# Kernel tuning notes

Hardware: AMD Instinct MI355X
Metric: run time of the kernel (lower is better)

## Reference

```python
import jax, jax.numpy as jnp
import numpy as np

VOCAB = 50257
D = 256
BATCH = 8


def setup_inputs() -> dict:
    key = jax.random.key(0)
    k1, k2, k3, k4, k5 = jax.random.split(key, 5)
    initial_ids = jax.random.randint(k1, (BATCH, 1), 0, VOCAB, dtype=jnp.int32)
    state = jax.random.normal(k2, (BATCH, D), dtype=jnp.float32)
    emb = jax.random.normal(k3, (VOCAB, D), dtype=jnp.float32) * 0.02
    W = jax.random.normal(k4, (D, VOCAB), dtype=jnp.float32) * 0.02
    U = jax.random.normal(k5, (D, D), dtype=jnp.float32) * 0.02
    return {"initial_ids": initial_ids, "state": state, "emb": emb,
            "W": W, "U": U, "beam_size": 32, "max_decode_length": 16}


def _logits_fn(ids, state, emb, W, U):
    # Stand-in for the external logits_fn: simple tanh-RNN cell + vocab projection.
    # ids: [b, beam, L], state: [b, beam, d]
    last = ids[:, :, -1]                                       # [b, beam]
    x = jnp.tanh(jnp.einsum('bkd,de->bke', state, U) + emb[last])  # [b, beam, d]
    token_scores = jax.nn.log_softmax(jnp.einsum('bkd,dv->bkv', x, W), axis=-1)
    return token_scores, x


def reference(initial_ids, state, emb, W, U, beam_size, max_decode_length):
    b = initial_ids.shape[0]
    vocab = W.shape[1]
    ids = initial_ids[:, None, :]                # [b, 1, L0]  (beam0 = 1)
    cache = state[:, None, :]                    # [b, 1, d]
    scores = jnp.zeros((b, 1), dtype=jnp.float32)
    for i in range(max_decode_length):           # unrolled, as in the TF original
        beam0 = ids.shape[1]
        token_scores, cache = _logits_fn(ids, cache, emb, W, U)   # [b,beam0,V]
        k = min(beam_size, beam0 * vocab)
        all_scores = (scores[:, :, None] + token_scores).reshape(b, beam0 * vocab)
        top_scores, top_ixs = jax.lax.top_k(all_scores, k)        # sorted, [b,k]
        top_beams = top_ixs // vocab                              # [b,k]
        top_tokens = top_ixs % vocab                              # [b,k]
        ids = jnp.take_along_axis(ids, top_beams[:, :, None], axis=1)
        ids = jnp.concatenate([ids, top_tokens[:, :, None].astype(ids.dtype)], axis=-1)
        cache = jnp.take_along_axis(cache, top_beams[:, :, None], axis=1)
        scores = top_scores
    return ids, scores
```

## Files before the change

### kernel.cpp

```cpp
#include <hip/hip_runtime.h>
#include <math.h>

#define B 8
#define D 256
#define V 50257
#define VP 50304
#define BEAM 32
#define STEPS 16
#define MAXLEN 17
#define FNEG_INF (-3.4e38f)
#define NG 1571
#define NLCAP 800
#define SLOTCAP 1600

struct SchedT {
    int nl, nops, nlev, root;
    int lvlStart[36];
    int leafOff[NLCAP];
    int leafN[NLCAP];
    int sA[NLCAP];
    int sB[NLCAP];
    int sD[NLCAP];
};

constexpr SchedT build_sched() {
    SchedT s{};
    int sOff[64] = {}, sN[64] = {}, sPh[64] = {};
    int vSlot[64] = {}, vLev[64] = {};
    int oA[NLCAP] = {}, oB[NLCAP] = {}, oD[NLCAP] = {}, oL[NLCAP] = {};
    int sp = 0, vp = 0, nl = 0, nops = 0;
    sOff[0] = 0; sN[0] = V; sPh[0] = 0; sp = 1;
    while (sp) {
        int i = sp - 1;
        int n = sN[i];
        if (n <= 128) {
            s.leafOff[nl] = sOff[i]; s.leafN[nl] = n;
            vSlot[vp] = nl; vLev[vp] = 0; ++vp; ++nl; --sp; continue;
        }
        int n2 = (n / 2) - ((n / 2) % 8);
        int ph = sPh[i];
        if (ph == 0)      { sPh[i] = 1; sOff[sp] = sOff[i];      sN[sp] = n2;     sPh[sp] = 0; ++sp; }
        else if (ph == 1) { sPh[i] = 2; sOff[sp] = sOff[i] + n2; sN[sp] = n - n2; sPh[sp] = 0; ++sp; }
        else {
            int bI = --vp; int aI = --vp;
            int lev = (vLev[aI] > vLev[bI] ? vLev[aI] : vLev[bI]) + 1;
            oA[nops] = vSlot[aI]; oB[nops] = vSlot[bI]; oD[nops] = NLCAP + nops; oL[nops] = lev;
            vSlot[vp] = NLCAP + nops; vLev[vp] = lev; ++vp; ++nops; --sp;
        }
    }
    s.nl = nl; s.nops = nops; s.root = vSlot[0];
    int maxl = 0;
    for (int k = 0; k < nops; ++k) if (oL[k] > maxl) maxl = oL[k];
    s.nlev = maxl;
    int cnt[36] = {};
    for (int k = 0; k < nops; ++k) cnt[oL[k]]++;
    int run = 0;
    s.lvlStart[0] = 0;
    for (int k = 1; k <= maxl; ++k) { s.lvlStart[k] = run; run += cnt[k]; cnt[k] = s.lvlStart[k]; }
    s.lvlStart[maxl + 1] = run;
    for (int k = 0; k < nops; ++k) { int p = cnt[oL[k]]++; s.sA[p] = oA[k]; s.sB[p] = oB[k]; s.sD[p] = oD[k]; }
    return s;
}

constexpr SchedT SCH = build_sched();
static_assert(SCH.nl <= NLCAP, "leaf overflow");
static_assert(SCH.nops <= NLCAP, "op overflow");
static_assert(SCH.nlev <= 34, "level overflow");
static_assert(SCH.root < SLOTCAP, "slot overflow");

__global__ void k_init(const int* __restrict__ initial_ids, const float* __restrict__ state,
                       float* __restrict__ cache, int* __restrict__ ids, float* __restrict__ scores) {
    int b = blockIdx.x, t = threadIdx.x;
    cache[b * D + t] = state[b * D + t];
    if (t == 0) { ids[b * MAXLEN] = initial_ids[b]; scores[b] = 0.f; }
}

__global__ __launch_bounds__(256) void k_embed(const float* __restrict__ cache, const int* __restrict__ ids,
                                               const float* __restrict__ emb, const float* __restrict__ U,
                                               float* __restrict__ x, int step) {
    int rr = blockIdx.x, j = threadIdx.x;
    __shared__ float sc[D];
    sc[j] = cache[rr * D + j];
    __syncthreads();
    int last = ids[rr * MAXLEN + step];
    float acc = 0.f;
    for (int d = 0; d < D; ++d)
        acc = __fadd_rn(acc, __fmul_rn(sc[d], U[d * D + j]));
    float pre = __fadd_rn(acc, emb[(size_t)last * D + j]);
    x[rr * D + j] = (float)tanh((double)pre);
}

__global__ __launch_bounds__(256) void k_trans(const float* __restrict__ x, float* __restrict__ xT) {
    __shared__ float tile[32][33];
    int t = threadIdx.x;
    int tx = t & 31, ty = t >> 5;
    int bx = blockIdx.x * 32, by = blockIdx.y * 32;
#pragma unroll
    for (int i = 0; i < 4; ++i)
        tile[ty + i * 8][tx] = x[(size_t)(by + ty + i * 8) * D + bx + tx];
    __syncthreads();
#pragma unroll
    for (int i = 0; i < 4; ++i)
        xT[(size_t)(bx + ty + i * 8) * 256 + by + tx] = tile[tx][ty + i * 8];
}

__global__ __launch_bounds__(256) void k_gemm(const float* __restrict__ xT, const float* __restrict__ W,
                                              float* __restrict__ L, int rows) {
    int t = threadIdx.x;
    int v = blockIdx.x * 256 + t;
    int r0 = blockIdx.y * 32;
    if (v >= V) return;
    float acc[32];
#pragma unroll
    for (int r = 0; r < 32; ++r) acc[r] = 0.f;
    for (int d = 0; d < D; ++d) {
        float w = W[(size_t)d * V + v];
        const float* xp = xT + d * 256 + r0;
#pragma unroll
        for (int r = 0; r < 32; ++r)
            acc[r] = __fadd_rn(acc[r], __fmul_rn(xp[r], w));
    }
#pragma unroll
    for (int r = 0; r < 32; ++r)
        if (r0 + r < rows) L[(size_t)(r0 + r) * VP + v] = acc[r];
}

__device__ __forceinline__ float Ev(const float* __restrict__ a, float m, int i) {
    return (float)exp((double)__fsub_rn(a[i], m));
}
__device__ float leaf_sum(const float* __restrict__ a, int n, float m) {
    if (n < 8) {
        if (n <= 0) return 0.f;
        float r = Ev(a, m, 0);
        for (int i = 1; i < n; ++i) r = __fadd_rn(r, Ev(a, m, i));
        return r;
    }
    float r0 = Ev(a,m,0), r1 = Ev(a,m,1), r2 = Ev(a,m,2), r3 = Ev(a,m,3);
    float r4 = Ev(a,m,4), r5 = Ev(a,m,5), r6 = Ev(a,m,6), r7 = Ev(a,m,7);
    int i;
    for (i = 8; i < n - (n % 8); i += 8) {
        r0 = __fadd_rn(r0, Ev(a,m,i+0)); r1 = __fadd_rn(r1, Ev(a,m,i+1));
        r2 = __fadd_rn(r2, Ev(a,m,i+2)); r3 = __fadd_rn(r3, Ev(a,m,i+3));
        r4 = __fadd_rn(r4, Ev(a,m,i+4)); r5 = __fadd_rn(r5, Ev(a,m,i+5));
        r6 = __fadd_rn(r6, Ev(a,m,i+6)); r7 = __fadd_rn(r7, Ev(a,m,i+7));
    }
    float res = __fadd_rn(__fadd_rn(__fadd_rn(r0, r1), __fadd_rn(r2, r3)),
                          __fadd_rn(__fadd_rn(r4, r5), __fadd_rn(r6, r7)));
    for (; i < n; ++i) res = __fadd_rn(res, Ev(a,m,i));
    return res;
}

__global__ __launch_bounds__(512) void k_post(const float* __restrict__ L, const float* __restrict__ scores,
                                              float* __restrict__ candV, int* __restrict__ candI) {
    int rr = blockIdx.x, t = threadIdx.x;
    const float* Lr = L + (size_t)rr * VP;
    __shared__ float red[512];
    __shared__ int ri[512];
    __shared__ float vals[SLOTCAP];
    __shared__ float gval[NG]; __shared__ int gidx[NG]; __shared__ unsigned gmask[NG];

    float mx = FNEG_INF;
    const float4* L4 = (const float4*)Lr;
    for (int i = t; i < V / 4; i += 512) {
        float4 p = L4[i];
        mx = fmaxf(mx, fmaxf(fmaxf(p.x, p.y), fmaxf(p.z, p.w)));
    }
    if (t == 0) mx = fmaxf(mx, Lr[V - 1]);
    red[t] = mx; __syncthreads();
    for (int o = 256; o > 0; o >>= 1) { if (t < o) red[t] = fmaxf(red[t], red[t + o]); __syncthreads(); }
    float m = red[0];

    for (int l = t; l < SCH.nl; l += 512)
        vals[l] = leaf_sum(Lr + SCH.leafOff[l], SCH.leafN[l], m);
    __syncthreads();
    for (int lev = 1; lev <= SCH.nlev; ++lev) {
        for (int i = SCH.lvlStart[lev] + t; i < SCH.lvlStart[lev + 1]; i += 512)
            vals[SCH.sD[i]] = __fadd_rn(vals[SCH.sA[i]], vals[SCH.sB[i]]);
        __syncthreads();
    }
    float lsf = (float)log((double)vals[SCH.root]);
    float sc = scores[rr];

    for (int g = t; g < NG; g += 512) {
        int c0 = g * 32;
        int lim = (V - c0) < 32 ? (V - c0) : 32;
        float bv = FNEG_INF; int bi = 0x7fffffff;
        for (int c = 0; c < lim; ++c) {
            int vtok = c0 + c;
            float val = __fadd_rn(sc, __fsub_rn(__fsub_rn(Lr[vtok], m), lsf));
            if (val > bv) { bv = val; bi = vtok; }
        }
        gval[g] = bv; gidx[g] = bi; gmask[g] = 0u;
    }
    __syncthreads();

    for (int it = 0; it < 32; ++it) {
        float bv = FNEG_INF; int bi = 0x7fffffff;
        for (int g = t; g < NG; g += 512) {
            float gv = gval[g]; int gi = gidx[g];
            if (gv > bv || (gv == bv && gi < bi)) { bv = gv; bi = gi; }
        }
        red[t] = bv; ri[t] = bi; __syncthreads();
        for (int o = 256; o > 0; o >>= 1) {
            if (t < o) {
                if (red[t + o] > red[t] || (red[t + o] == red[t] && ri[t + o] < ri[t])) { red[t] = red[t + o]; ri[t] = ri[t + o]; }
            }
            __syncthreads();
        }
        int wcol = ri[0]; int wg = wcol >> 5;
        if (t == 0) {
            candV[rr * 32 + it] = red[0];
            candI[rr * 32 + it] = wcol;
            gmask[wg] |= (1u << (wcol & 31));
        }
        __syncthreads();
        if (t < 32) {
            int col = wg * 32 + t;
            unsigned msk = gmask[wg];
            bool live = (col < V) && !((msk >> t) & 1u);
            float val = live ? __fadd_rn(sc, __fsub_rn(__fsub_rn(Lr[col], m), lsf)) : FNEG_INF;
            int ix = live ? col : 0x7fffffff;
            for (int o = 16; o > 0; o >>= 1) {
                float v2 = __shfl_down(val, o, 32);
                int i2 = __shfl_down(ix, o, 32);
                if (v2 > val || (v2 == val && i2 < ix)) { val = v2; ix = i2; }
            }
            if (t == 0) { gval[wg] = val; gidx[wg] = ix; }
        }
        __syncthreads();
    }
}

__global__ __launch_bounds__(256) void k_merge(const float* __restrict__ candV, const int* __restrict__ candI,
                                               float* __restrict__ scoresNxt,
                                               const int* __restrict__ idsCur, int* __restrict__ idsNxt,
                                               const float* __restrict__ x, float* __restrict__ cacheNxt,
                                               int beam0, int step) {
    int b = blockIdx.x, t = threadIdx.x;
    int n = beam0 * BEAM;
    __shared__ float mval[BEAM * BEAM]; __shared__ int mbeam[BEAM * BEAM]; __shared__ int mtok[BEAM * BEAM];
    __shared__ float rv[256]; __shared__ int rk[256]; __shared__ int rs[256];
    __shared__ float wval[BEAM]; __shared__ int wbeam[BEAM]; __shared__ int wtok[BEAM];

    for (int i = t; i < n; i += 256) {
        int beam = i >> 5;
        int rr = b * beam0 + beam;
        mval[i] = candV[rr * BEAM + (i & 31)];
        mbeam[i] = beam;
        mtok[i] = candI[rr * BEAM + (i & 31)];
    }
    __syncthreads();

    for (int it = 0; it < BEAM; ++it) {
        float bv = FNEG_INF; int bk = 0x7fffffff; int bs = -1;
        for (int i = t; i < n; i += 256) {
            float v = mval[i];
            int gi = mbeam[i] * V + mtok[i];
            if (v > bv || (v == bv && gi < bk)) { bv = v; bk = gi; bs = i; }
        }
        rv[t] = bv; rk[t] = bk; rs[t] = bs; __syncthreads();
        for (int o = 128; o > 0; o >>= 1) {
            if (t < o) {
                if (rv[t + o] > rv[t] || (rv[t + o] == rv[t] && rk[t + o] < rk[t])) {
                    rv[t] = rv[t + o]; rk[t] = rk[t + o]; rs[t] = rs[t + o];
                }
            }
            __syncthreads();
        }
        if (t == 0) {
            int w = rs[0];
            wval[it] = rv[0]; wbeam[it] = mbeam[w]; wtok[it] = mtok[w];
            mval[w] = FNEG_INF;
        }
        __syncthreads();
    }

    if (t < BEAM) {
        scoresNxt[b * BEAM + t] = wval[t];
        int src = b * beam0 + wbeam[t];
        for (int u = 0; u <= step; ++u)
            idsNxt[(b * BEAM + t) * MAXLEN + u] = idsCur[src * MAXLEN + u];
        idsNxt[(b * BEAM + t) * MAXLEN + step + 1] = wtok[t];
    }
    __syncthreads();
    for (int j = 0; j < BEAM; ++j) {
        int src = b * beam0 + wbeam[j];
        cacheNxt[(size_t)(b * BEAM + j) * D + t] = x[(size_t)src * D + t];
    }
}

__global__ void k_out(const int* __restrict__ ids, const float* __restrict__ scores, float* __restrict__ out) {
    int t = blockIdx.x * 256 + threadIdx.x;
    const int NI = B * BEAM * MAXLEN;
    if (t < NI) out[t] = (float)ids[t];
    else if (t < NI + B * BEAM) out[t] = scores[t - NI];
}

extern "C" void kernel_launch(void* const* d_in, const int* in_sizes, int n_in,
                              void* d_out, int out_size, void* d_ws, size_t ws_size,
                              hipStream_t stream) {
    const int* initial_ids = (const int*)d_in[0];
    const float* state = (const float*)d_in[1];
    const float* emb = (const float*)d_in[2];
    const float* W = (const float*)d_in[3];
    const float* U = (const float*)d_in[4];

    char* ws = (char*)d_ws;
    size_t off = 0;
    float* L = (float*)(ws + off);       off += (size_t)256 * VP * 4;
    float* x = (float*)(ws + off);       off += 256 * D * 4;
    float* xT = (float*)(ws + off);      off += 256 * D * 4;
    float* cacheA = (float*)(ws + off);  off += 256 * D * 4;
    float* cacheB = (float*)(ws + off);  off += 256 * D * 4;
    float* scoresA = (float*)(ws + off); off += 256 * 4;
    float* scoresB = (float*)(ws + off); off += 256 * 4;
    int* idsA = (int*)(ws + off);        off += 256 * MAXLEN * 4;
    int* idsB = (int*)(ws + off);        off += 256 * MAXLEN * 4;
    float* candV = (float*)(ws + off);   off += 256 * 32 * 4;
    int* candI = (int*)(ws + off);       off += 256 * 32 * 4;

    if (ws_size < off) return;

    k_init<<<B, 256, 0, stream>>>(initial_ids, state, cacheA, idsA, scoresA);

    float* cCur = cacheA; float* cNxt = cacheB;
    float* sCur = scoresA; float* sNxt = scoresB;
    int* iCur = idsA; int* iNxt = idsB;

    for (int step = 0; step < STEPS; ++step) {
        int beam0 = (step == 0) ? 1 : BEAM;
        int rows = B * beam0;

        k_embed<<<rows, 256, 0, stream>>>(cCur, iCur, emb, U, x, step);

        dim3 gt(8, 8);
        k_trans<<<gt, 256, 0, stream>>>(x, xT);

        dim3 g((V + 255) / 256, (rows + 31) / 32);
        k_gemm<<<g, 256, 0, stream>>>(xT, W, L, rows);

        k_post<<<rows, 512, 0, stream>>>(L, sCur, candV, candI);
        k_merge<<<B, 256, 0, stream>>>(candV, candI, sNxt, iCur, iNxt, x, cNxt, beam0, step);

        float* tf; int* ti;
        tf = cCur; cCur = cNxt; cNxt = tf;
        tf = sCur; sCur = sNxt; sNxt = tf;
        ti = iCur; iCur = iNxt; iNxt = ti;
    }

    k_out<<<(B * BEAM * MAXLEN + B * BEAM + 255) / 256, 256, 0, stream>>>(iCur, sCur, (float*)d_out);
}
```

Baseline: 5.116 ms.

## Fuse row max into GEMM and use wave-parallel top-k selection in post

The GEMM epilogue now reduces per-256-column segment maxima with wave shuffles and writes them to a segMax buffer, so k_post no longer rescans each logit row to find the max. The softmax leaf sums are split across 8-lane clusters instead of one thread per leaf. Group argmax is computed with shuffles across 32 lanes rather than serial 32-element loops. A two-level supergroup index lets the 32-iteration top-k loop run in a single wave without block-wide syncs. This targets k_post's serial scans and barrier cost, in exchange for extra shuffle work and a store in the GEMM and a more complex selection path.

Measured after the change: 5.558 ms. 8.7% more time.

```diff
diff --git a/kernel.cpp b/kernel.cpp
--- a/kernel.cpp
+++ b/kernel.cpp
@@ -10,11 +10,15 @@
 #define MAXLEN 17
 #define FNEG_INF (-3.4e38f)
 #define NG 1571
+#define NSG 50
+#define NSEG 197
 #define NLCAP 800
 #define SLOTCAP 1600
 
+static_assert((V + 255) / 256 == NSEG, "NSEG mismatch");
+
 struct SchedT {
-    int nl, nops, nlev, root;
+    int nl, nops, nlev, root, minLeaf;
     int lvlStart[36];
     int leafOff[NLCAP];
     int leafN[NLCAP];
@@ -29,12 +33,14 @@
     int vSlot[64] = {}, vLev[64] = {};
     int oA[NLCAP] = {}, oB[NLCAP] = {}, oD[NLCAP] = {}, oL[NLCAP] = {};
     int sp = 0, vp = 0, nl = 0, nops = 0;
+    s.minLeaf = 1 << 30;
     sOff[0] = 0; sN[0] = V; sPh[0] = 0; sp = 1;
     while (sp) {
         int i = sp - 1;
         int n = sN[i];
         if (n <= 128) {
             s.leafOff[nl] = sOff[i]; s.leafN[nl] = n;
+            if (n < s.minLeaf) s.minLeaf = n;
             vSlot[vp] = nl; vLev[vp] = 0; ++vp; ++nl; --sp; continue;
         }
         int n2 = (n / 2) - ((n / 2) % 8);
@@ -67,6 +73,7 @@
 static_assert(SCH.nops <= NLCAP, "op overflow");
 static_assert(SCH.nlev <= 34, "level overflow");
 static_assert(SCH.root < SLOTCAP, "slot overflow");
+static_assert(SCH.minLeaf >= 8, "leaf < 8 would break 8-lane cluster sum");
 
 __global__ void k_init(const int* __restrict__ initial_ids, const float* __restrict__ state,
                        float* __restrict__ cache, int* __restrict__ ids, float* __restrict__ scores) {
@@ -105,16 +112,16 @@
 }
 
 __global__ __launch_bounds__(256) void k_gemm(const float* __restrict__ xT, const float* __restrict__ W,
-                                              float* __restrict__ L, int rows) {
+                                              float* __restrict__ L, float* __restrict__ segMax, int rows) {
     int t = threadIdx.x;
     int v = blockIdx.x * 256 + t;
     int r0 = blockIdx.y * 32;
-    if (v >= V) return;
+    bool vok = (v < V);
     float acc[32];
 #pragma unroll
     for (int r = 0; r < 32; ++r) acc[r] = 0.f;
     for (int d = 0; d < D; ++d) {
-        float w = W[(size_t)d * V + v];
+        float w = vok ? W[(size_t)d * V + v] : 0.f;
         const float* xp = xT + d * 256 + r0;
 #pragma unroll
         for (int r = 0; r < 32; ++r)
@@ -122,56 +129,63 @@
     }
 #pragma unroll
     for (int r = 0; r < 32; ++r)
-        if (r0 + r < rows) L[(size_t)(r0 + r) * VP + v] = acc[r];
+        if (vok && r0 + r < rows) L[(size_t)(r0 + r) * VP + v] = acc[r];
+
+    __shared__ float wmax[4][32];
+    int wave = t >> 6, lane = t & 63;
+#pragma unroll
+    for (int r = 0; r < 32; ++r) {
+        float mv = vok ? acc[r] : FNEG_INF;
+#pragma unroll
+        for (int o = 1; o < 64; o <<= 1) mv = fmaxf(mv, __shfl_xor(mv, o));
+        if (lane == 0) wmax[wave][r] = mv;
+    }
+    __syncthreads();
+    if (t < 32 && r0 + t < rows) {
+        float mv = fmaxf(fmaxf(wmax[0][t], wmax[1][t]), fmaxf(wmax[2][t], wmax[3][t]));
+        segMax[(size_t)(r0 + t) * NSEG + blockIdx.x] = mv;
+    }
 }
 
 __device__ __forceinline__ float Ev(const float* __restrict__ a, float m, int i) {
     return (float)exp((double)__fsub_rn(a[i], m));
 }
-__device__ float leaf_sum(const float* __restrict__ a, int n, float m) {
-    if (n < 8) {
-        if (n <= 0) return 0.f;
-        float r = Ev(a, m, 0);
-        for (int i = 1; i < n; ++i) r = __fadd_rn(r, Ev(a, m, i));
-        return r;
-    }
-    float r0 = Ev(a,m,0), r1 = Ev(a,m,1), r2 = Ev(a,m,2), r3 = Ev(a,m,3);
-    float r4 = Ev(a,m,4), r5 = Ev(a,m,5), r6 = Ev(a,m,6), r7 = Ev(a,m,7);
-    int i;
-    for (i = 8; i < n - (n % 8); i += 8) {
-        r0 = __fadd_rn(r0, Ev(a,m,i+0)); r1 = __fadd_rn(r1, Ev(a,m,i+1));
-        r2 = __fadd_rn(r2, Ev(a,m,i+2)); r3 = __fadd_rn(r3, Ev(a,m,i+3));
-        r4 = __fadd_rn(r4, Ev(a,m,i+4)); r5 = __fadd_rn(r5, Ev(a,m,i+5));
-        r6 = __fadd_rn(r6, Ev(a,m,i+6)); r7 = __fadd_rn(r7, Ev(a,m,i+7));
-    }
-    float res = __fadd_rn(__fadd_rn(__fadd_rn(r0, r1), __fadd_rn(r2, r3)),
-                          __fadd_rn(__fadd_rn(r4, r5), __fadd_rn(r6, r7)));
-    for (; i < n; ++i) res = __fadd_rn(res, Ev(a,m,i));
-    return res;
-}
-
-__global__ __launch_bounds__(512) void k_post(const float* __restrict__ L, const float* __restrict__ scores,
+
+__global__ __launch_bounds__(512) void k_post(const float* __restrict__ L, const float* __restrict__ segMax,
+                                              const float* __restrict__ scores,
                                               float* __restrict__ candV, int* __restrict__ candI) {
     int rr = blockIdx.x, t = threadIdx.x;
     const float* Lr = L + (size_t)rr * VP;
-    __shared__ float red[512];
-    __shared__ int ri[512];
+    __shared__ float mS;
     __shared__ float vals[SLOTCAP];
     __shared__ float gval[NG]; __shared__ int gidx[NG]; __shared__ unsigned gmask[NG];
-
-    float mx = FNEG_INF;
-    const float4* L4 = (const float4*)Lr;
-    for (int i = t; i < V / 4; i += 512) {
-        float4 p = L4[i];
-        mx = fmaxf(mx, fmaxf(fmaxf(p.x, p.y), fmaxf(p.z, p.w)));
-    }
-    if (t == 0) mx = fmaxf(mx, Lr[V - 1]);
-    red[t] = mx; __syncthreads();
-    for (int o = 256; o > 0; o >>= 1) { if (t < o) red[t] = fmaxf(red[t], red[t + o]); __syncthreads(); }
-    float m = red[0];
-
-    for (int l = t; l < SCH.nl; l += 512)
-        vals[l] = leaf_sum(Lr + SCH.leafOff[l], SCH.leafN[l], m);
+    __shared__ float sgval[64]; __shared__ int sgtok[64]; __shared__ int sggrp[64];
+
+    if (t < 64) {
+        float mv = FNEG_INF;
+        for (int s = t; s < NSEG; s += 64) mv = fmaxf(mv, segMax[(size_t)rr * NSEG + s]);
+#pragma unroll
+        for (int o = 1; o < 64; o <<= 1) mv = fmaxf(mv, __shfl_xor(mv, o));
+        if (t == 0) mS = mv;
+    }
+    __syncthreads();
+    float m = mS;
+
+    int cl = t >> 3, j = t & 7;
+    for (int l = cl; l < SCH.nl; l += 64) {
+        int off = SCH.leafOff[l], n = SCH.leafN[l];
+        int n8 = n - (n % 8);
+        float r = Ev(Lr, m, off + j);
+        for (int i = 8; i < n8; i += 8) r = __fadd_rn(r, Ev(Lr, m, off + i + j));
+        float s1 = __fadd_rn(r,  __shfl_xor(r, 1));
+        float s2 = __fadd_rn(s1, __shfl_xor(s1, 2));
+        float s3 = __fadd_rn(s2, __shfl_xor(s2, 4));
+        if (j == 0) {
+            float res = s3;
+            for (int i = n8; i < n; ++i) res = __fadd_rn(res, Ev(Lr, m, off + i));
+            vals[l] = res;
+        }
+    }
     __syncthreads();
     for (int lev = 1; lev <= SCH.nlev; ++lev) {
         for (int i = SCH.lvlStart[lev] + t; i < SCH.lvlStart[lev + 1]; i += 512)
@@ -181,53 +195,87 @@
     float lsf = (float)log((double)vals[SCH.root]);
     float sc = scores[rr];
 
-    for (int g = t; g < NG; g += 512) {
-        int c0 = g * 32;
-        int lim = (V - c0) < 32 ? (V - c0) : 32;
-        float bv = FNEG_INF; int bi = 0x7fffffff;
-        for (int c = 0; c < lim; ++c) {
-            int vtok = c0 + c;
-            float val = __fadd_rn(sc, __fsub_rn(__fsub_rn(Lr[vtok], m), lsf));
-            if (val > bv) { bv = val; bi = vtok; }
-        }
-        gval[g] = bv; gidx[g] = bi; gmask[g] = 0u;
-    }
-    __syncthreads();
+    int wv = t >> 6, ln = t & 63;
+    for (int g2 = wv * 2; g2 < NG; g2 += 16) {
+        int g = g2 + (ln >> 5);
+        int col = g2 * 32 + ln;
+        bool liveg = (g < NG);
+        bool live = liveg && (col < V);
+        float val = live ? __fadd_rn(sc, __fsub_rn(__fsub_rn(Lr[col], m), lsf)) : FNEG_INF;
+        int ix = live ? col : 0x7fffffff;
+#pragma unroll
+        for (int o = 1; o < 32; o <<= 1) {
+            float v2 = __shfl_xor(val, o);
+            int i2 = __shfl_xor(ix, o);
+            if (v2 > val || (v2 == val && i2 < ix)) { val = v2; ix = i2; }
+        }
+        if (liveg && (ln & 31) == 0) { gval[g] = val; gidx[g] = ix; gmask[g] = 0u; }
+    }
+    __syncthreads();
+
+    for (int s2 = wv * 2; s2 < NSG; s2 += 16) {
+        int s = s2 + (ln >> 5);
+        int g = s2 * 32 + ln;
+        bool lives = (s < NSG);
+        bool live = lives && (g < NG);
+        float val = live ? gval[g] : FNEG_INF;
+        int tok = live ? gidx[g] : 0x7fffffff;
+        int grp = live ? g : -1;
+#pragma unroll
+        for (int o = 1; o < 32; o <<= 1) {
+            float v2 = __shfl_xor(val, o);
+            int t2 = __shfl_xor(tok, o);
+            int g3 = __shfl_xor(grp, o);
+            if (v2 > val || (v2 == val && t2 < tok)) { val = v2; tok = t2; grp = g3; }
+        }
+        if (lives && (ln & 31) == 0) { sgval[s] = val; sgtok[s] = tok; sggrp[s] = grp; }
+    }
+    __syncthreads();
+    if (t >= 64) return;
 
     for (int it = 0; it < 32; ++it) {
-        float bv = FNEG_INF; int bi = 0x7fffffff;
-        for (int g = t; g < NG; g += 512) {
-            float gv = gval[g]; int gi = gidx[g];
-            if (gv > bv || (gv == bv && gi < bi)) { bv = gv; bi = gi; }
-        }
-        red[t] = bv; ri[t] = bi; __syncthreads();
-        for (int o = 256; o > 0; o >>= 1) {
-            if (t < o) {
-                if (red[t + o] > red[t] || (red[t + o] == red[t] && ri[t + o] < ri[t])) { red[t] = red[t + o]; ri[t] = ri[t + o]; }
-            }
-            __syncthreads();
-        }
-        int wcol = ri[0]; int wg = wcol >> 5;
+        float val = (t < NSG) ? sgval[t] : FNEG_INF;
+        int tok = (t < NSG) ? sgtok[t] : 0x7fffffff;
+        int grp = (t < NSG) ? sggrp[t] : -1;
+#pragma unroll
+        for (int o = 1; o < 64; o <<= 1) {
+            float v2 = __shfl_xor(val, o);
+            int t2 = __shfl_xor(tok, o);
+            int g3 = __shfl_xor(grp, o);
+            if (v2 > val || (v2 == val && t2 < tok)) { val = v2; tok = t2; grp = g3; }
+        }
+        int gw = grp, tw = tok;
+        unsigned newmask = gmask[gw] | (1u << (tw & 31));
         if (t == 0) {
-            candV[rr * 32 + it] = red[0];
-            candI[rr * 32 + it] = wcol;
-            gmask[wg] |= (1u << (wcol & 31));
-        }
-        __syncthreads();
-        if (t < 32) {
-            int col = wg * 32 + t;
-            unsigned msk = gmask[wg];
-            bool live = (col < V) && !((msk >> t) & 1u);
-            float val = live ? __fadd_rn(sc, __fsub_rn(__fsub_rn(Lr[col], m), lsf)) : FNEG_INF;
-            int ix = live ? col : 0x7fffffff;
-            for (int o = 16; o > 0; o >>= 1) {
-                float v2 = __shfl_down(val, o, 32);
-                int i2 = __shfl_down(ix, o, 32);
-                if (v2 > val || (v2 == val && i2 < ix)) { val = v2; ix = i2; }
-            }
-            if (t == 0) { gval[wg] = val; gidx[wg] = ix; }
-        }
-        __syncthreads();
+            candV[rr * 32 + it] = val;
+            candI[rr * 32 + it] = tw;
+            gmask[gw] = newmask;
+        }
+        int col = gw * 32 + (t & 31);
+        bool live = (col < V) && !((newmask >> (t & 31)) & 1u);
+        float nv = live ? __fadd_rn(sc, __fsub_rn(__fsub_rn(Lr[col], m), lsf)) : FNEG_INF;
+        int nix = live ? col : 0x7fffffff;
+#pragma unroll
+        for (int o = 1; o < 32; o <<= 1) {
+            float v2 = __shfl_xor(nv, o);
+            int i2 = __shfl_xor(nix, o);
+            if (v2 > nv || (v2 == nv && i2 < nix)) { nv = v2; nix = i2; }
+        }
+        if (t == 0) { gval[gw] = nv; gidx[gw] = nix; }
+        int s = gw >> 5;
+        int gg = s * 32 + (t & 31);
+        bool lv = (gg < NG);
+        float sv = lv ? gval[gg] : FNEG_INF;
+        int st = lv ? gidx[gg] : 0x7fffffff;
+        int sg2 = lv ? gg : -1;
+#pragma unroll
+        for (int o = 1; o < 32; o <<= 1) {
+            float v2 = __shfl_xor(sv, o);
+            int t2 = __shfl_xor(st, o);
+            int g3 = __shfl_xor(sg2, o);
+            if (v2 > sv || (v2 == sv && t2 < st)) { sv = v2; st = t2; sg2 = g3; }
+        }
+        if (t == 0) { sgval[s] = sv; sgtok[s] = st; sggrp[s] = sg2; }
     }
 }
 
@@ -318,6 +366,7 @@
     int* idsB = (int*)(ws + off);        off += 256 * MAXLEN * 4;
     float* candV = (float*)(ws + off);   off += 256 * 32 * 4;
     int* candI = (int*)(ws + off);       off += 256 * 32 * 4;
+    float* segMax = (float*)(ws + off);  off += (size_t)256 * NSEG * 4;
 
     if (ws_size < off) return;
 
@@ -336,10 +385,10 @@
         dim3 gt(8, 8);
         k_trans<<<gt, 256, 0, stream>>>(x, xT);
 
-        dim3 g((V + 255) / 256, (rows + 31) / 32);
-        k_gemm<<<g, 256, 0, stream>>>(xT, W, L, rows);
-
-        k_post<<<rows, 512, 0, stream>>>(L, sCur, candV, candI);
+        dim3 g(NSEG, (rows + 31) / 32);
+        k_gemm<<<g, 256, 0, stream>>>(xT, W, L, segMax, rows);
+
+        k_post<<<rows, 512, 0, stream>>>(L, segMax, sCur, candV, candI);
         k_merge<<<B, 256, 0, stream>>>(candV, candI, sNxt, iCur, iNxt, x, cNxt, beam0, step);
 
         float* tf; int* ti;
```
